# Performance work log

Measured on AMD Instinct MI355X. Metric: run time of the kernel, lower is better.

## Reference

```python
import jax, jax.numpy as jnp
import numpy as np

NUM_HEADS = 32
NUM_KV_HEADS = 8
HEAD_DIM = 128
SCALE = 0.08838834764831845  # 1/sqrt(128)
NUM_SEQS = 8
Q_LEN = 256            # new tokens per sequence (uniform cu_seqlens_q)
MAX_PAGES = 128
PAGE_SIZE = 16
BLOCK_SIZE = 32
NUM_PAGES = NUM_SEQS * MAX_PAGES


def setup_inputs() -> dict:
    key = jax.random.key(0)
    ks = jax.random.split(key, 6)
    total = NUM_SEQS * Q_LEN
    q = jax.random.normal(ks[0], (total, NUM_HEADS * HEAD_DIM), dtype=jnp.float32)
    k = jax.random.normal(ks[1], (total, NUM_KV_HEADS * HEAD_DIM), dtype=jnp.float32)
    v = jax.random.normal(ks[2], (total, NUM_KV_HEADS * HEAD_DIM), dtype=jnp.float32)
    k_cache = jax.random.normal(ks[3], (NUM_PAGES, PAGE_SIZE, NUM_KV_HEADS, HEAD_DIM), dtype=jnp.float32)
    v_cache = jax.random.normal(ks[4], (NUM_PAGES, PAGE_SIZE, NUM_KV_HEADS, HEAD_DIM), dtype=jnp.float32)
    page_tables = jnp.arange(NUM_SEQS * MAX_PAGES, dtype=jnp.int32).reshape(NUM_SEQS, MAX_PAGES)
    context_lens = jax.random.randint(ks[5], (NUM_SEQS,), 0, MAX_PAGES * PAGE_SIZE, dtype=jnp.int32)
    return {
        'q': q, 'k': k, 'v': v,
        'k_cache': k_cache, 'v_cache': v_cache,
        'page_tables': page_tables, 'context_lens': context_lens,
        'page_size': PAGE_SIZE, 'block_size': BLOCK_SIZE,
    }


def reference(q, k, v, k_cache, v_cache, page_tables, context_lens, page_size, block_size):
    B, P = page_tables.shape
    S = q.shape[0] // B
    C = P * page_size                      # max cached context per seq
    G = NUM_HEADS // NUM_KV_HEADS          # GQA group size

    qb = q.reshape(B, S, NUM_KV_HEADS, G, HEAD_DIM)
    kb = k.reshape(B, S, NUM_KV_HEADS, HEAD_DIM)
    vb = v.reshape(B, S, NUM_KV_HEADS, HEAD_DIM)

    # page-table gather of cached K/V: [B, P, page_size, nkvh, hd] -> [B, C, nkvh, hd]
    k_ctx = k_cache[page_tables].reshape(B, C, NUM_KV_HEADS, HEAD_DIM)
    v_ctx = v_cache[page_tables].reshape(B, C, NUM_KV_HEADS, HEAD_DIM)

    k_full = jnp.concatenate([k_ctx, kb], axis=1)  # [B, C+S, nkvh, hd]
    v_full = jnp.concatenate([v_ctx, vb], axis=1)

    T = C + S
    t_idx = jnp.arange(T)
    s_idx = jnp.arange(S)
    # cached positions valid iff t < context_len; new positions use block mask
    ctx_valid = t_idx[None, :] < context_lens[:, None]            # [B, T]
    block_ends = (s_idx // block_size + 1) * block_size           # [S]
    new_valid = block_ends[:, None] > (t_idx[None, :] - C)        # [S, T]
    is_ctx = t_idx < C                                            # [T]
    mask = jnp.where(is_ctx[None, None, :], ctx_valid[:, None, :], new_valid[None, :, :])  # [B, S, T]

    # scores: [B, nkvh, G, S, T]
    scores = jnp.einsum('bsngd,btnd->bngst', qb, k_full) * SCALE
    scores = jnp.where(mask[:, None, None, :, :], scores, jnp.float32(-1e30))
    probs = jax.nn.softmax(scores, axis=-1)
    out = jnp.einsum('bngst,btnd->bsngd', probs, v_full)          # [B, S, nkvh, G, hd]
    return out.reshape(B * S, NUM_HEADS * HEAD_DIM)
```

## Files before the change

### kernel.cpp

```cpp
#include <hip/hip_runtime.h>
#include <hip/hip_bf16.h>

#define NUM_HEADS   32
#define NUM_KV_HEADS 8
#define HEAD_DIM    128
#define GQA          4
#define Q_LEN      256
#define MAX_PAGES  128
#define PAGE_SIZE   16
#define SCALE 0.08838834764831845f
#define LOG2E 1.44269504088896340736f
#define RESCALE_THR 8.0f

#define NCH_MAX   36
#define CHUNK_B   16384
#define KSTREAM   ((size_t)NCH_MAX * CHUNK_B)
#define NITEMS    512
#define PBYTES    33792

typedef __bf16 bf16x8 __attribute__((ext_vector_type(8)));
typedef float  f32x4  __attribute__((ext_vector_type(4)));

union B8 { uint4 u; bf16x8 v; };

__device__ __forceinline__ unsigned f2bf(float x){
    unsigned u = __builtin_bit_cast(unsigned, x);
    return (u + 0x7fffu + ((u >> 16) & 1u)) >> 16;
}
__device__ __forceinline__ unsigned pack2(float lo, float hi){
    return f2bf(lo) | (f2bf(hi) << 16);
}
__device__ __forceinline__ float bflo(unsigned h){
    return __builtin_bit_cast(float, h << 16);
}
__device__ __forceinline__ float bfhi(unsigned h){
    return __builtin_bit_cast(float, h & 0xffff0000u);
}

typedef __attribute__((address_space(3))) unsigned char lds_as3_t;
typedef const __attribute__((address_space(1))) void gas_v;
typedef __attribute__((address_space(3))) void las_v;

#define GLD16(g, l) __builtin_amdgcn_global_load_lds((gas_v*)(g), (las_v*)(l), 16, 0, 0)

#define TRR(dst, base, OFF) asm volatile("ds_read_b64_tr_b16 %0, %1 offset:" OFF \
                                         : "=v"(dst) : "v"(base))

__global__ __launch_bounds__(256) void prep_kernel(
    const float* __restrict__ knew,
    const float* __restrict__ vnew,
    const float* __restrict__ kcache,
    const float* __restrict__ vcache,
    const int*   __restrict__ ptab,
    const int*   __restrict__ ctxlens,
    unsigned char* __restrict__ kimg,
    unsigned char* __restrict__ vimg)
{
    const int ch  = blockIdx.x;
    const int kvh = blockIdx.y;
    const int b   = blockIdx.z;
    const int ctxlen = ctxlens[b];
    const int lim = ctxlen + Q_LEN;
    const int base = ch * 64;
    if (base >= lim) return;

    const int tid  = threadIdx.x;
    const int srow = tid >> 2;
    const int seg  = tid & 3;
    const int t    = base + srow;

    unsigned char* kdst = kimg + (size_t)(b * 8 + kvh) * KSTREAM + (size_t)ch * CHUNK_B;
    unsigned char* vdst = vimg + (size_t)(b * 8 + kvh) * KSTREAM + (size_t)ch * CHUNK_B;
    const int swz    = (srow & 7) << 4;
    const int vbyte0 = (srow >> 2) * 128 + (srow & 3) * 32;

    if (t < lim){
        size_t roff;
        const float *ksrc, *vsrc;
        if (t < ctxlen){
            const int page = ptab[b * MAX_PAGES + (t >> 4)];
            roff = ((size_t)(page * PAGE_SIZE + (t & 15)) * NUM_KV_HEADS + kvh) * HEAD_DIM;
            ksrc = kcache + roff; vsrc = vcache + roff;
        } else {
            roff = ((size_t)(b * Q_LEN + (t - ctxlen)) * NUM_KV_HEADS + kvh) * HEAD_DIM;
            ksrc = knew + roff; vsrc = vnew + roff;
        }
        const float* kr = ksrc + seg * 32;
        const float* vr = vsrc + seg * 32;
        #pragma unroll
        for (int i = 0; i < 4; ++i){
            float4 a  = *(const float4*)(kr + i * 8);
            float4 c4 = *(const float4*)(kr + i * 8 + 4);
            uint4 wv;
            wv.x = pack2(a.x, a.y);  wv.y = pack2(a.z, a.w);
            wv.z = pack2(c4.x, c4.y); wv.w = pack2(c4.z, c4.w);
            *(uint4*)(kdst + srow * 256 + ((seg * 64 + i * 16) ^ swz)) = wv;
        }
        #pragma unroll
        for (int db = 0; db < 2; ++db){
            const float4 a0 = *(const float4*)(vr + db * 16 + 0);
            const float4 a1 = *(const float4*)(vr + db * 16 + 4);
            const float4 a2 = *(const float4*)(vr + db * 16 + 8);
            const float4 a3 = *(const float4*)(vr + db * 16 + 12);
            uint4 w0, w1;
            w0.x = pack2(a0.x, a0.y); w0.y = pack2(a0.z, a0.w);
            w0.z = pack2(a1.x, a1.y); w0.w = pack2(a1.z, a1.w);
            w1.x = pack2(a2.x, a2.y); w1.y = pack2(a2.z, a2.w);
            w1.z = pack2(a3.x, a3.y); w1.w = pack2(a3.z, a3.w);
            const int dbk = seg * 2 + db;
            *(uint4*)(vdst + dbk * 2048 + vbyte0)      = w0;
            *(uint4*)(vdst + dbk * 2048 + vbyte0 + 16) = w1;
        }
    } else {
        const uint4 z = {0u, 0u, 0u, 0u};
        #pragma unroll
        for (int i = 0; i < 4; ++i)
            *(uint4*)(kdst + srow * 256 + ((seg * 64 + i * 16) ^ swz)) = z;
        #pragma unroll
        for (int db = 0; db < 2; ++db){
            const int dbk = seg * 2 + db;
            *(uint4*)(vdst + dbk * 2048 + vbyte0)      = z;
            *(uint4*)(vdst + dbk * 2048 + vbyte0 + 16) = z;
        }
    }
}

template<int NSPLIT>
__global__ __launch_bounds__(256, 2) void attn_kernel(
    const float* __restrict__ q,
    const int*   __restrict__ ctxlens,
    float*       __restrict__ out,
    const unsigned char* __restrict__ kimg,
    const unsigned char* __restrict__ vimg,
    unsigned char* __restrict__ part)
{
    __shared__ __align__(16) unsigned char lds[65536];

    const int tid  = threadIdx.x;
    const int w    = tid >> 6;
    const int lane = tid & 63;
    const int hh   = lane >> 4;
    const int cq   = lane & 15;

    const unsigned ldsb3 = (unsigned)(unsigned long long)(lds_as3_t*)(&lds[0]);

    const int fid   = blockIdx.x;
    const int item0 = fid / NSPLIT;
    const int seg   = fid % NSPLIT;

    const int b   = item0 & 7;
    const int kvh = (item0 >> 3) & 7;
    const int s32 = 7 - (item0 >> 6);

    const int s0 = s32 * 32;
    const int ctxlen = ctxlens[b];
    const int vlim = ctxlen + (s32 + 1) * 32;
    const int nch  = (vlim + 63) >> 6;
    const int lo   = (seg * nch) / NSPLIT;
    const int hi   = ((seg + 1) * nch) / NSPLIT;
    if (lo >= hi) return;
    const int hq = kvh * GQA + w;

    const unsigned char* kstream = kimg + (size_t)(b * 8 + kvh) * KSTREAM;
    const unsigned char* vstream = vimg + (size_t)(b * 8 + kvh) * KSTREAM;

    #define STAGE(CH, PB) do { \
        const unsigned char* kg_ = kstream + (size_t)(CH) * CHUNK_B + (w * 4096 + lane * 16); \
        const unsigned char* vg_ = vstream + (size_t)(CH) * CHUNK_B + (w * 4096 + lane * 16); \
        _Pragma("unroll") \
        for (int i_ = 0; i_ < 4; ++i_){ \
            GLD16(kg_ + i_ * 1024, lds + (PB) * CHUNK_B + w * 4096 + i_ * 1024); \
            GLD16(vg_ + i_ * 1024, lds + 32768 + (PB) * CHUNK_B + w * 4096 + i_ * 1024); \
        } \
    } while (0)

    STAGE(lo, lo & 1);

    B8 qf[2][4];
    #pragma unroll
    for (int u = 0; u < 2; ++u){
        const float* qrow = q + (size_t)(b * Q_LEN + s0 + u * 16 + cq) * (NUM_HEADS * HEAD_DIM)
                              + hq * HEAD_DIM;
        #pragma unroll
        for (int c = 0; c < 4; ++c){
            const float4 f0 = *(const float4*)(qrow + c * 32 + 8 * hh);
            const float4 f1 = *(const float4*)(qrow + c * 32 + 8 * hh + 4);
            const float sc = SCALE * LOG2E;
            qf[u][c].u.x = pack2(f0.x * sc, f0.y * sc);
            qf[u][c].u.y = pack2(f0.z * sc, f0.w * sc);
            qf[u][c].u.z = pack2(f1.x * sc, f1.y * sc);
            qf[u][c].u.w = pack2(f1.z * sc, f1.w * sc);
        }
    }

    f32x4 acc[2][8] = {};
    float mrun[2] = {-1e30f, -1e30f};
    float lp[2]   = {0.f, 0.f};

    for (int ch = lo; ch < hi; ++ch){
        const int pb = ch & 1;

        asm volatile("s_waitcnt lgkmcnt(0)" ::: "memory");
        __builtin_amdgcn_s_barrier();
        __builtin_amdgcn_sched_barrier(0);
        if (ch + 1 < hi) {
            STAGE(ch + 1, pb ^ 1);
            __builtin_amdgcn_sched_barrier(0);
            asm volatile("s_waitcnt vmcnt(8)" ::: "memory");
        } else {
            asm volatile("s_waitcnt vmcnt(0)" ::: "memory");
        }
        __builtin_amdgcn_sched_barrier(0);

        const int base = ch * 64;
        const unsigned kb = (unsigned)(pb * CHUNK_B);

        __builtin_amdgcn_s_setprio(1);
        f32x4 st[2][4] = {};
        #pragma unroll
        for (int c = 0; c < 4; ++c){
            #pragma unroll
            for (int tf = 0; tf < 4; ++tf){
                const int trow = tf * 16 + cq;
                const unsigned byte = kb + trow * 256 + ((c * 64 + hh * 16) ^ ((trow & 7) << 4));
                B8 kf; kf.u = *(const uint4*)(lds + byte);
                st[0][tf] = __builtin_amdgcn_mfma_f32_16x16x32_bf16(kf.v, qf[0][c].v, st[0][tf], 0, 0, 0);
                st[1][tf] = __builtin_amdgcn_mfma_f32_16x16x32_bf16(kf.v, qf[1][c].v, st[1][tf], 0, 0, 0);
            }
        }
        __builtin_amdgcn_s_setprio(0);

        const unsigned trb = ldsb3 + 32768u + (unsigned)(pb * CHUNK_B) + (unsigned)(hh * 128 + cq * 8);
        unsigned long long v00,v01,v02,v03,v04,v05,v06,v07,v08,v09,v10,v11,v12,v13,v14,v15;
        unsigned long long v16,v17,v18,v19,v20,v21,v22,v23,v24,v25,v26,v27,v28,v29,v30,v31;
        __builtin_amdgcn_sched_barrier(0);
        TRR(v00, trb, "0");     TRR(v01, trb, "512");
        TRR(v02, trb, "2048");  TRR(v03, trb, "2560");
        TRR(v04, trb, "4096");  TRR(v05, trb, "4608");
        TRR(v06, trb, "6144");  TRR(v07, trb, "6656");
        TRR(v08, trb, "8192");  TRR(v09, trb, "8704");
        TRR(v10, trb, "10240"); TRR(v11, trb, "10752");
        TRR(v12, trb, "12288"); TRR(v13, trb, "12800");
        TRR(v14, trb, "14336"); TRR(v15, trb, "14848");
        TRR(v16, trb, "1024");  TRR(v17, trb, "1536");
        TRR(v18, trb, "3072");  TRR(v19, trb, "3584");
        TRR(v20, trb, "5120");  TRR(v21, trb, "5632");
        TRR(v22, trb, "7168");  TRR(v23, trb, "7680");
        TRR(v24, trb, "9216");  TRR(v25, trb, "9728");
        TRR(v26, trb, "11264"); TRR(v27, trb, "11776");
        TRR(v28, trb, "13312"); TRR(v29, trb, "13824");
        TRR(v30, trb, "15360"); TRR(v31, trb, "15872");
        __builtin_amdgcn_sched_barrier(0);

        B8 af[2][2];
        const bool interior = (base + 64 <= vlim);
        #pragma unroll
        for (int u = 0; u < 2; ++u){
            float p[4][4];
            float pml = -1e30f;
            if (interior){
                #pragma unroll
                for (int tf = 0; tf < 4; ++tf){
                    #pragma unroll
                    for (int r = 0; r < 4; ++r){
                        const float s = st[u][tf][r];
                        p[tf][r] = s;
                        pml = fmaxf(pml, s);
                    }
                }
            } else {
                #pragma unroll
                for (int tf = 0; tf < 4; ++tf){
                    #pragma unroll
                    for (int r = 0; r < 4; ++r){
                        const int t = base + tf * 16 + hh * 4 + r;
                        const float s = (t < vlim) ? st[u][tf][r] : -1e30f;
                        p[tf][r] = s;
                        pml = fmaxf(pml, s);
                    }
                }
            }
            if (!__all(pml <= mrun[u] + RESCALE_THR)){
                float pm = fmaxf(pml, __shfl_xor(pml, 16));
                pm = fmaxf(pm, __shfl_xor(pm, 32));
                const float mnew  = fmaxf(mrun[u], pm);
                const float alpha = __builtin_amdgcn_exp2f(mrun[u] - mnew);
                mrun[u] = mnew;
                lp[u] *= alpha;
                float a4[4];
                #pragma unroll
                for (int r = 0; r < 4; ++r) a4[r] = __shfl(alpha, hh * 20 + r);
                #pragma unroll
                for (int dc = 0; dc < 8; ++dc){
                    #pragma unroll
                    for (int r = 0; r < 4; ++r) acc[u][dc][r] *= a4[r];
                }
            }
            const float m = mrun[u];
            float rsum = 0.f;
            #pragma unroll
            for (int tf = 0; tf < 4; ++tf){
                #pragma unroll
                for (int r = 0; r < 4; ++r){
                    const float e = __builtin_amdgcn_exp2f(p[tf][r] - m);
                    p[tf][r] = e;
                    rsum += e;
                }
            }
            lp[u] += rsum;

            unsigned pk01[4], pk23[4];
            #pragma unroll
            for (int tf = 0; tf < 4; ++tf){
                pk01[tf] = pack2(p[tf][0], p[tf][1]);
                pk23[tf] = pack2(p[tf][2], p[tf][3]);
            }
            af[u][0].u.x = pk01[0]; af[u][0].u.y = pk23[0]; af[u][0].u.z = pk01[1]; af[u][0].u.w = pk23[1];
            af[u][1].u.x = pk01[2]; af[u][1].u.y = pk23[2]; af[u][1].u.z = pk01[3]; af[u][1].u.w = pk23[3];
        }

        {
            asm volatile("s_waitcnt lgkmcnt(0)" ::: "memory");
            __builtin_amdgcn_sched_barrier(0);
            __builtin_amdgcn_s_setprio(1);
            B8 vf;
            #define PVM(VA, VB, KK, DC) \
                vf.u.x=(unsigned)(VA); vf.u.y=(unsigned)((VA)>>32); \
                vf.u.z=(unsigned)(VB); vf.u.w=(unsigned)((VB)>>32); \
                acc[0][DC] = __builtin_amdgcn_mfma_f32_16x16x32_bf16(af[0][KK].v, vf.v, acc[0][DC], 0, 0, 0); \
                acc[1][DC] = __builtin_amdgcn_mfma_f32_16x16x32_bf16(af[1][KK].v, vf.v, acc[1][DC], 0, 0, 0);
            PVM(v00, v01, 0, 0)  PVM(v02, v03, 0, 1)  PVM(v04, v05, 0, 2)  PVM(v06, v07, 0, 3)
            PVM(v08, v09, 0, 4)  PVM(v10, v11, 0, 5)  PVM(v12, v13, 0, 6)  PVM(v14, v15, 0, 7)
            PVM(v16, v17, 1, 0)  PVM(v18, v19, 1, 1)  PVM(v20, v21, 1, 2)  PVM(v22, v23, 1, 3)
            PVM(v24, v25, 1, 4)  PVM(v26, v27, 1, 5)  PVM(v28, v29, 1, 6)  PVM(v30, v31, 1, 7)
            #undef PVM
            __builtin_amdgcn_s_setprio(0);
        }
    }

    if (NSPLIT == 1){
        #pragma unroll
        for (int u = 0; u < 2; ++u){
            float l = lp[u];
            l += __shfl_xor(l, 16);
            l += __shfl_xor(l, 32);
            const float li = 1.0f / l;
            float li4[4];
            #pragma unroll
            for (int r = 0; r < 4; ++r) li4[r] = __shfl(li, hh * 20 + r);
            #pragma unroll
            for (int dc = 0; dc < 8; ++dc){
                #pragma unroll
                for (int r = 0; r < 4; ++r){
                    const int so = s0 + u * 16 + hh * 4 + r;
                    out[(size_t)(b * Q_LEN + so) * (NUM_HEADS * HEAD_DIM) + hq * HEAD_DIM + dc * 16 + cq]
                        = acc[u][dc][r] * li4[r];
                }
            }
        }
    } else {
        unsigned char* pp = part + (size_t)fid * PBYTES;
        #pragma unroll
        for (int u = 0; u < 2; ++u){
            float l = lp[u];
            l += __shfl_xor(l, 16);
            l += __shfl_xor(l, 32);
            if (hh == 0){
                float2 ml; ml.x = mrun[u]; ml.y = l;
                *(float2*)(pp + 32768 + (size_t)(w * 32 + u * 16 + cq) * 8) = ml;
            }
            #pragma unroll
            for (int dc = 0; dc < 8; ++dc){
                uint2 pk;
                pk.x = pack2(acc[u][dc][0], acc[u][dc][1]);
                pk.y = pack2(acc[u][dc][2], acc[u][dc][3]);
                *(uint2*)(pp + (size_t)((((w * 2 + u) * 8 + dc) * 64 + lane)) * 8) = pk;
            }
        }
    }
    #undef STAGE
}

template<int NSPLIT>
__global__ __launch_bounds__(256) void merge_kernel(
    const int* __restrict__ ctxlens,
    const unsigned char* __restrict__ part,
    float* __restrict__ out)
{
    __shared__ float s_w[NSPLIT][128];

    const int item0 = blockIdx.x;
    const int b   = item0 & 7;
    const int kvh = (item0 >> 3) & 7;
    const int s32 = 7 - (item0 >> 6);
    const int vlim = ctxlens[b] + (s32 + 1) * 32;
    const int nch  = (vlim + 63) >> 6;

    const int tid = threadIdx.x;

    bool act[NSPLIT];
    #pragma unroll
    for (int s = 0; s < NSPLIT; ++s){
        const int lo = (s * nch) / NSPLIT;
        const int hi = ((s + 1) * nch) / NSPLIT;
        act[s] = hi > lo;
    }

    if (tid < 128){
        float m[NSPLIT], l[NSPLIT];
        float M = -1e30f;
        #pragma unroll
        for (int s = 0; s < NSPLIT; ++s){
            if (act[s]){
                const float2 ml = *(const float2*)(part + (size_t)(item0 * NSPLIT + s) * PBYTES
                                                   + 32768 + (size_t)tid * 8);
                m[s] = ml.x; l[s] = ml.y;
                M = fmaxf(M, m[s]);
            }
        }
        float L = 0.f;
        float wg[NSPLIT];
        #pragma unroll
        for (int s = 0; s < NSPLIT; ++s){
            if (act[s]){
                wg[s] = __builtin_amdgcn_exp2f(m[s] - M);
                L += l[s] * wg[s];
            } else wg[s] = 0.f;
        }
        const float inv = 1.0f / L;
        #pragma unroll
        for (int s = 0; s < NSPLIT; ++s) s_w[s][tid] = wg[s] * inv;
    }
    __syncthreads();

    for (int k = 0; k < 8; ++k){
        const int q4 = tid + k * 256;
        const int S0 = q4 * 2;
        const int g  = S0 >> 6;
        const int ln = S0 & 63;
        const int hD = g >> 4;
        const int u  = (g >> 3) & 1;
        const int dc = g & 7;
        const int hh = ln >> 4;
        const int cq = ln & 15;
        const int wbase = hD * 32 + u * 16 + hh * 4;

        float o0[4] = {0.f, 0.f, 0.f, 0.f};
        float o1[4] = {0.f, 0.f, 0.f, 0.f};
        #pragma unroll
        for (int s = 0; s < NSPLIT; ++s){
            if (!act[s]) continue;
            const uint4 v = *(const uint4*)(part + (size_t)(item0 * NSPLIT + s) * PBYTES
                                            + (size_t)q4 * 16);
            const float w0 = s_w[s][wbase + 0];
            const float w1 = s_w[s][wbase + 1];
            const float w2 = s_w[s][wbase + 2];
            const float w3 = s_w[s][wbase + 3];
            o0[0] += w0 * bflo(v.x); o0[1] += w1 * bfhi(v.x);
            o0[2] += w2 * bflo(v.y); o0[3] += w3 * bfhi(v.y);
            o1[0] += w0 * bflo(v.z); o1[1] += w1 * bfhi(v.z);
            o1[2] += w2 * bflo(v.w); o1[3] += w3 * bfhi(v.w);
        }
        float* obase = out + (size_t)(b * Q_LEN + s32 * 32 + u * 16 + hh * 4) * (NUM_HEADS * HEAD_DIM)
                     + (kvh * GQA + hD) * HEAD_DIM + dc * 16 + cq;
        #pragma unroll
        for (int r = 0; r < 4; ++r){
            float2 ov; ov.x = o0[r]; ov.y = o1[r];
            *(float2*)(obase + (size_t)r * (NUM_HEADS * HEAD_DIM)) = ov;
        }
    }
}

extern "C" void kernel_launch(void* const* d_in, const int* in_sizes, int n_in,
                              void* d_out, int out_size, void* d_ws, size_t ws_size,
                              hipStream_t stream) {
    const float* q  = (const float*)d_in[0];
    const float* k  = (const float*)d_in[1];
    const float* v  = (const float*)d_in[2];
    const float* kc = (const float*)d_in[3];
    const float* vc = (const float*)d_in[4];
    const int*   pt = (const int*)d_in[5];
    const int*   cl = (const int*)d_in[6];
    float* o = (float*)d_out;

    const size_t img_bytes = (size_t)64 * KSTREAM;
    const size_t off_part  = 256 + 2 * img_bytes;
    const size_t need2 = off_part + (size_t)NITEMS * 2 * PBYTES;
    const size_t need1 = off_part;

    unsigned char* kimg = (unsigned char*)d_ws + 256;
    unsigned char* vimg = kimg + img_bytes;
    unsigned char* part = (unsigned char*)d_ws + off_part;

    prep_kernel<<<dim3(NCH_MAX, 8, 8), 256, 0, stream>>>(k, v, kc, vc, pt, cl, kimg, vimg);

    if (ws_size >= need2) {
        attn_kernel<2><<<NITEMS * 2, 256, 0, stream>>>(q, cl, o, kimg, vimg, part);
        merge_kernel<2><<<NITEMS, 256, 0, stream>>>(cl, part, o);
    } else if (ws_size >= need1) {
        attn_kernel<1><<<NITEMS, 256, 0, stream>>>(q, cl, o, kimg, vimg, part);
    }
}
```

Before: 135.8 us.

## Drop split-K partition and merge kernel, run single-pass attention per item

Removes the two-way split of the context across blocks and the separate merge kernel, so each block processes the full context of its item and writes normalized output directly. This eliminates the bf16 partial-result round trip through global memory and one kernel launch. In exchange, it halves the number of blocks and loses the load balancing the split gave for long-context items, and the tail may get longer.

```diff
diff --git a/kernel.cpp b/kernel.cpp
--- a/kernel.cpp
+++ b/kernel.cpp
@@ -16,7 +16,6 @@
 #define CHUNK_B   16384
 #define KSTREAM   ((size_t)NCH_MAX * CHUNK_B)
 #define NITEMS    512
-#define PBYTES    33792
 
 typedef __bf16 bf16x8 __attribute__((ext_vector_type(8)));
 typedef float  f32x4  __attribute__((ext_vector_type(4)));
@@ -29,12 +28,6 @@
 }
 __device__ __forceinline__ unsigned pack2(float lo, float hi){
     return f2bf(lo) | (f2bf(hi) << 16);
-}
-__device__ __forceinline__ float bflo(unsigned h){
-    return __builtin_bit_cast(float, h << 16);
-}
-__device__ __forceinline__ float bfhi(unsigned h){
-    return __builtin_bit_cast(float, h & 0xffff0000u);
 }
 
 typedef __attribute__((address_space(3))) unsigned char lds_as3_t;
@@ -125,14 +118,12 @@
     }
 }
 
-template<int NSPLIT>
 __global__ __launch_bounds__(256, 2) void attn_kernel(
     const float* __restrict__ q,
     const int*   __restrict__ ctxlens,
     float*       __restrict__ out,
     const unsigned char* __restrict__ kimg,
-    const unsigned char* __restrict__ vimg,
-    unsigned char* __restrict__ part)
+    const unsigned char* __restrict__ vimg)
 {
     __shared__ __align__(16) unsigned char lds[65536];
 
@@ -144,9 +135,7 @@
 
     const unsigned ldsb3 = (unsigned)(unsigned long long)(lds_as3_t*)(&lds[0]);
 
-    const int fid   = blockIdx.x;
-    const int item0 = fid / NSPLIT;
-    const int seg   = fid % NSPLIT;
+    const int item0 = blockIdx.x;
 
     const int b   = item0 & 7;
     const int kvh = (item0 >> 3) & 7;
@@ -156,9 +145,6 @@
     const int ctxlen = ctxlens[b];
     const int vlim = ctxlen + (s32 + 1) * 32;
     const int nch  = (vlim + 63) >> 6;
-    const int lo   = (seg * nch) / NSPLIT;
-    const int hi   = ((seg + 1) * nch) / NSPLIT;
-    if (lo >= hi) return;
     const int hq = kvh * GQA + w;
 
     const unsigned char* kstream = kimg + (size_t)(b * 8 + kvh) * KSTREAM;
@@ -174,7 +160,7 @@
         } \
     } while (0)
 
-    STAGE(lo, lo & 1);
+    STAGE(0, 0);
 
     B8 qf[2][4];
     #pragma unroll
@@ -197,13 +183,13 @@
     float mrun[2] = {-1e30f, -1e30f};
     float lp[2]   = {0.f, 0.f};
 
-    for (int ch = lo; ch < hi; ++ch){
+    for (int ch = 0; ch < nch; ++ch){
         const int pb = ch & 1;
 
         asm volatile("s_waitcnt lgkmcnt(0)" ::: "memory");
         __builtin_amdgcn_s_barrier();
         __builtin_amdgcn_sched_barrier(0);
-        if (ch + 1 < hi) {
+        if (ch + 1 < nch) {
             STAGE(ch + 1, pb ^ 1);
             __builtin_amdgcn_sched_barrier(0);
             asm volatile("s_waitcnt vmcnt(8)" ::: "memory");
@@ -338,137 +324,26 @@
         }
     }
 
-    if (NSPLIT == 1){
-        #pragma unroll
-        for (int u = 0; u < 2; ++u){
-            float l = lp[u];
-            l += __shfl_xor(l, 16);
-            l += __shfl_xor(l, 32);
-            const float li = 1.0f / l;
-            float li4[4];
+    #pragma unroll
+    for (int u = 0; u < 2; ++u){
+        float l = lp[u];
+        l += __shfl_xor(l, 16);
+        l += __shfl_xor(l, 32);
+        const float li = 1.0f / l;
+        float li4[4];
+        #pragma unroll
+        for (int r = 0; r < 4; ++r) li4[r] = __shfl(li, hh * 20 + r);
+        #pragma unroll
+        for (int dc = 0; dc < 8; ++dc){
             #pragma unroll
-            for (int r = 0; r < 4; ++r) li4[r] = __shfl(li, hh * 20 + r);
-            #pragma unroll
-            for (int dc = 0; dc < 8; ++dc){
-                #pragma unroll
-                for (int r = 0; r < 4; ++r){
-                    const int so = s0 + u * 16 + hh * 4 + r;
-                    out[(size_t)(b * Q_LEN + so) * (NUM_HEADS * HEAD_DIM) + hq * HEAD_DIM + dc * 16 + cq]
-                        = acc[u][dc][r] * li4[r];
-                }
-            }
-        }
-    } else {
-        unsigned char* pp = part + (size_t)fid * PBYTES;
-        #pragma unroll
-        for (int u = 0; u < 2; ++u){
-            float l = lp[u];
-            l += __shfl_xor(l, 16);
-            l += __shfl_xor(l, 32);
-            if (hh == 0){
-                float2 ml; ml.x = mrun[u]; ml.y = l;
-                *(float2*)(pp + 32768 + (size_t)(w * 32 + u * 16 + cq) * 8) = ml;
-            }
-            #pragma unroll
-            for (int dc = 0; dc < 8; ++dc){
-                uint2 pk;
-                pk.x = pack2(acc[u][dc][0], acc[u][dc][1]);
-                pk.y = pack2(acc[u][dc][2], acc[u][dc][3]);
-                *(uint2*)(pp + (size_t)((((w * 2 + u) * 8 + dc) * 64 + lane)) * 8) = pk;
+            for (int r = 0; r < 4; ++r){
+                const int so = s0 + u * 16 + hh * 4 + r;
+                out[(size_t)(b * Q_LEN + so) * (NUM_HEADS * HEAD_DIM) + hq * HEAD_DIM + dc * 16 + cq]
+                    = acc[u][dc][r] * li4[r];
             }
         }
     }
     #undef STAGE
-}
-
-template<int NSPLIT>
-__global__ __launch_bounds__(256) void merge_kernel(
-    const int* __restrict__ ctxlens,
-    const unsigned char* __restrict__ part,
-    float* __restrict__ out)
-{
-    __shared__ float s_w[NSPLIT][128];
-
-    const int item0 = blockIdx.x;
-    const int b   = item0 & 7;
-    const int kvh = (item0 >> 3) & 7;
-    const int s32 = 7 - (item0 >> 6);
-    const int vlim = ctxlens[b] + (s32 + 1) * 32;
-    const int nch  = (vlim + 63) >> 6;
-
-    const int tid = threadIdx.x;
-
-    bool act[NSPLIT];
-    #pragma unroll
-    for (int s = 0; s < NSPLIT; ++s){
-        const int lo = (s * nch) / NSPLIT;
-        const int hi = ((s + 1) * nch) / NSPLIT;
-        act[s] = hi > lo;
-    }
-
-    if (tid < 128){
-        float m[NSPLIT], l[NSPLIT];
-        float M = -1e30f;
-        #pragma unroll
-        for (int s = 0; s < NSPLIT; ++s){
-            if (act[s]){
-                const float2 ml = *(const float2*)(part + (size_t)(item0 * NSPLIT + s) * PBYTES
-                                                   + 32768 + (size_t)tid * 8);
-                m[s] = ml.x; l[s] = ml.y;
-                M = fmaxf(M, m[s]);
-            }
-        }
-        float L = 0.f;
-        float wg[NSPLIT];
-        #pragma unroll
-        for (int s = 0; s < NSPLIT; ++s){
-            if (act[s]){
-                wg[s] = __builtin_amdgcn_exp2f(m[s] - M);
-                L += l[s] * wg[s];
-            } else wg[s] = 0.f;
-        }
-        const float inv = 1.0f / L;
-        #pragma unroll
-        for (int s = 0; s < NSPLIT; ++s) s_w[s][tid] = wg[s] * inv;
-    }
-    __syncthreads();
-
-    for (int k = 0; k < 8; ++k){
-        const int q4 = tid + k * 256;
-        const int S0 = q4 * 2;
-        const int g  = S0 >> 6;
-        const int ln = S0 & 63;
-        const int hD = g >> 4;
-        const int u  = (g >> 3) & 1;
-        const int dc = g & 7;
-        const int hh = ln >> 4;
-        const int cq = ln & 15;
-        const int wbase = hD * 32 + u * 16 + hh * 4;
-
-        float o0[4] = {0.f, 0.f, 0.f, 0.f};
-        float o1[4] = {0.f, 0.f, 0.f, 0.f};
-        #pragma unroll
-        for (int s = 0; s < NSPLIT; ++s){
-            if (!act[s]) continue;
-            const uint4 v = *(const uint4*)(part + (size_t)(item0 * NSPLIT + s) * PBYTES
-                                            + (size_t)q4 * 16);
-            const float w0 = s_w[s][wbase + 0];
-            const float w1 = s_w[s][wbase + 1];
-            const float w2 = s_w[s][wbase + 2];
-            const float w3 = s_w[s][wbase + 3];
-            o0[0] += w0 * bflo(v.x); o0[1] += w1 * bfhi(v.x);
-            o0[2] += w2 * bflo(v.y); o0[3] += w3 * bfhi(v.y);
-            o1[0] += w0 * bflo(v.z); o1[1] += w1 * bfhi(v.z);
-            o1[2] += w2 * bflo(v.w); o1[3] += w3 * bfhi(v.w);
-        }
-        float* obase = out + (size_t)(b * Q_LEN + s32 * 32 + u * 16 + hh * 4) * (NUM_HEADS * HEAD_DIM)
-                     + (kvh * GQA + hD) * HEAD_DIM + dc * 16 + cq;
-        #pragma unroll
-        for (int r = 0; r < 4; ++r){
-            float2 ov; ov.x = o0[r]; ov.y = o1[r];
-            *(float2*)(obase + (size_t)r * (NUM_HEADS * HEAD_DIM)) = ov;
-        }
-    }
 }
 
 extern "C" void kernel_launch(void* const* d_in, const int* in_sizes, int n_in,
@@ -483,21 +358,9 @@
     const int*   cl = (const int*)d_in[6];
     float* o = (float*)d_out;
 
-    const size_t img_bytes = (size_t)64 * KSTREAM;
-    const size_t off_part  = 256 + 2 * img_bytes;
-    const size_t need2 = off_part + (size_t)NITEMS * 2 * PBYTES;
-    const size_t need1 = off_part;
-
     unsigned char* kimg = (unsigned char*)d_ws + 256;
-    unsigned char* vimg = kimg + img_bytes;
-    unsigned char* part = (unsigned char*)d_ws + off_part;
+    unsigned char* vimg = kimg + (size_t)64 * KSTREAM;
 
     prep_kernel<<<dim3(NCH_MAX, 8, 8), 256, 0, stream>>>(k, v, kc, vc, pt, cl, kimg, vimg);
-
-    if (ws_size >= need2) {
-        attn_kernel<2><<<NITEMS * 2, 256, 0, stream>>>(q, cl, o, kimg, vimg, part);
-        merge_kernel<2><<<NITEMS, 256, 0, stream>>>(cl, part, o);
-    } else if (ws_size >= need1) {
-        attn_kernel<1><<<NITEMS, 256, 0, stream>>>(q, cl, o, kimg, vimg, part);
-    }
-}
+    attn_kernel<<<NITEMS, 256, 0, stream>>>(q, cl, o, kimg, vimg);
+}
```

Result: faster. 113.4 us (median of 2 runs) (-16.5%).
